# Optimization experiments

Measured on AMD Instinct MI355X. Metric: run time of the kernel, lower is better.

## Reference

```python
import jax, jax.numpy as jnp
import numpy as np

D, H, F, Z = 768, 12, 2048, 100   # d_model, nhead, dim_feedforward, d_z
NL = 2                            # num enc layers == num dec layers
RATIO = 0.05                      # filter_ratio
EPS = 1e-5


def _ln(x, g, b):
    m = x.mean(-1, keepdims=True)
    v = ((x - m) ** 2).mean(-1, keepdims=True)
    return (x - m) / jnp.sqrt(v + EPS) * g + b


def _mha(x, bias, qkv_w, qkv_b, out_w, out_b):
    # x: [N, L, D] (torch seq-first: seq=N responses, batch=L token positions)
    # bias: [L, N] float key-padding mask, ADDED to logits (torch float-mask semantics)
    N, L, _ = x.shape
    hd = D // H
    qkv = jnp.einsum('nld,ed->nle', x, qkv_w) + qkv_b
    q, k, v = jnp.split(qkv, 3, axis=-1)
    q = q.reshape(N, L, H, hd)
    k = k.reshape(N, L, H, hd)
    v = v.reshape(N, L, H, hd)
    scores = jnp.einsum('nlhd,mlhd->lhnm', q, k) / jnp.sqrt(jnp.float32(hd))
    scores = scores + bias[:, None, None, :]
    attn = jax.nn.softmax(scores, axis=-1)
    o = jnp.einsum('lhnm,mlhd->nlhd', attn, v).reshape(N, L, D)
    return o @ out_w.T + out_b


def _stack(x, bias, p):
    qkv_w, qkv_b, out_w, out_b, g1, b1, w1, c1, w2, c2, g2, b2 = p
    for i in range(NL):  # post-norm TransformerEncoderLayer, relu FFN, eval (no dropout)
        a = _mha(x, bias, qkv_w[i], qkv_b[i], out_w[i], out_b[i])
        x = _ln(x + a, g1[i], b1[i])
        f = jax.nn.relu(x @ w1[i].T + c1[i]) @ w2[i].T + c2[i]
        x = _ln(x + f, g2[i], b2[i])
    return x


def _anomaly_scores(emb, msk, enc_p, dec_p, pe_w, pe_b, pd_w, pd_b):
    bias = msk.T  # [L, N]
    h = _stack(emb, bias, enc_p)
    z = jnp.tanh(h @ pe_w.T + pe_b)
    zd = jnp.tanh(z @ pd_w.T + pd_b)
    d = _stack(zd, bias, dec_p)
    # per-response MSE between mean decoded and mean input embedding, summed over D
    return ((d.mean(axis=1) - emb.mean(axis=1)) ** 2).sum(-1)


def _forward(tree_lens, inputs_embeds, attention_mask, enc_p, dec_p, pe_w, pe_b, pd_w, pd_b):
    B, T, L, _ = inputs_embeds.shape
    tls = np.asarray(tree_lens)
    n_resp = tls - 1
    # pack ragged replies: rows 1..tree_len-1 of every tree -> [Ntot, L, D]
    b_idx = np.concatenate([np.full(n, b) for b, n in enumerate(n_resp)])
    t_idx = np.concatenate([np.arange(1, tl) for tl in tls])
    reply = inputs_embeds[b_idx, t_idx]
    masks = attention_mask[b_idx, t_idx]
    s = _anomaly_scores(reply, masks, enc_p, dec_p, pe_w, pe_b, pd_w, pd_b)  # [Ntot]
    Ntot = s.shape[0]
    # original: rank_idx = global_argsort filtered to indices < n_resp[b] (min is always 0)
    # == argsort of the FIRST n_resp[b] packed scores (faithful to the source's indexing)
    masked = jnp.where(jnp.arange(Ntot)[None, :] < jnp.asarray(n_resp)[:, None],
                       s[None, :], jnp.inf)
    order = jnp.argsort(masked, axis=1)[:, :T - 1]  # [B, T-1]
    n_ext = np.maximum(np.floor(n_resp * RATIO).astype(np.int64), 1)
    sel = np.arange(T - 1)[None, :] < n_ext[:, None]          # [B, T-1]
    selj = jnp.asarray(sel)
    node_idx = jnp.where(selj, order + 1, 0)                  # pad slots reuse src (node 0)
    node_full = jnp.concatenate([jnp.zeros((B, 1), node_idx.dtype), node_idx], axis=1)
    brow = jnp.arange(B)[:, None]
    new_emb = inputs_embeds[brow, node_full]                  # [B, T, L, D]
    valid = jnp.asarray(np.concatenate([np.ones((B, 1), bool), sel], axis=1)
                        ).astype(attention_mask.dtype)
    new_msk = attention_mask[brow, node_full] * valid[:, :, None]  # pad rows get zero mask
    ohidx = jnp.where(selj, order + 1, T)                     # dump masked scatters to col T
    oh = jnp.zeros((B, T + 1), jnp.int32).at[brow, ohidx].set(1)[:, :T].at[:, 0].set(1)
    ext_mask = jnp.repeat(oh[:, :, None], L, axis=2).reshape(B, T * L)
    new_tree_lens = jnp.asarray(1 + n_ext, dtype=jnp.int32)
    n_ext_adv = 0
    return oh, ext_mask, n_ext_adv, new_tree_lens, new_emb, new_msk


def setup_inputs() -> dict:
    B, T, L = 16, 32, 64
    key = jax.random.key(0)
    ks = list(jax.random.split(key, 4))
    inp = {
        'tree_lens': jax.random.randint(ks[0], (B,), T // 2, T + 1),
        'inputs_embeds': jax.random.normal(ks[1], (B, T, L, D), jnp.float32),
        'attention_mask': jnp.ones((B, T, L), jnp.float32),
    }
    kit = iter(jax.random.split(ks[2], 32))
    def w(shape):
        return jax.random.normal(next(kit), (NL,) + shape, jnp.float32) * 0.02
    for pre in ('enc', 'dec'):
        inp[pre + '_qkv_w'] = w((3 * D, D)); inp[pre + '_qkv_b'] = jnp.zeros((NL, 3 * D))
        inp[pre + '_out_w'] = w((D, D));     inp[pre + '_out_b'] = jnp.zeros((NL, D))
        inp[pre + '_ln1_g'] = jnp.ones((NL, D)); inp[pre + '_ln1_b'] = jnp.zeros((NL, D))
        inp[pre + '_w1'] = w((F, D)); inp[pre + '_c1'] = jnp.zeros((NL, F))
        inp[pre + '_w2'] = w((D, F)); inp[pre + '_c2'] = jnp.zeros((NL, D))
        inp[pre + '_ln2_g'] = jnp.ones((NL, D)); inp[pre + '_ln2_b'] = jnp.zeros((NL, D))
    inp['pe_w'] = jax.random.normal(next(kit), (Z, D), jnp.float32) * 0.02
    inp['pe_b'] = jnp.zeros((Z,), jnp.float32)
    inp['pd_w'] = jax.random.normal(next(kit), (D, Z), jnp.float32) * 0.02
    inp['pd_b'] = jnp.zeros((D,), jnp.float32)
    return inp


def reference(tree_lens, inputs_embeds, attention_mask,
              enc_qkv_w, enc_qkv_b, enc_out_w, enc_out_b, enc_ln1_g, enc_ln1_b,
              enc_w1, enc_c1, enc_w2, enc_c2, enc_ln2_g, enc_ln2_b,
              dec_qkv_w, dec_qkv_b, dec_out_w, dec_out_b, dec_ln1_g, dec_ln1_b,
              dec_w1, dec_c1, dec_w2, dec_c2, dec_ln2_g, dec_ln2_b,
              pe_w, pe_b, pd_w, pd_b):
    enc_p = (enc_qkv_w, enc_qkv_b, enc_out_w, enc_out_b, enc_ln1_g, enc_ln1_b,
             enc_w1, enc_c1, enc_w2, enc_c2, enc_ln2_g, enc_ln2_b)
    dec_p = (dec_qkv_w, dec_qkv_b, dec_out_w, dec_out_b, dec_ln1_g, dec_ln1_b,
             dec_w1, dec_c1, dec_w2, dec_c2, dec_ln2_g, dec_ln2_b)
    return _forward(tree_lens, inputs_embeds, attention_mask, enc_p, dec_p,
                    pe_w, pe_b, pd_w, pd_b)
```

## Files before the change

kernel.cpp:

```cpp
#include <hip/hip_runtime.h>
#include <hip/hip_bf16.h>
#include <math.h>


#define B_  16
#define T_  32
#define L_  64
#define D_  768
#define H_  12
#define F_  2048
#define ZR_ 100
#define NP_ 512
#define EPS_ 1e-5f

#define MI_NTOT  0
#define MI_NRESP 8
#define MI_OFF   32
#define MI_BIDX  64
#define MI_TIDX  576
#define MI_NODE  1088

#define WS_BIAS2 2048
#define WS_EMEAN 34816
#define WS_S     428032
#define WS_WST   428544
#define WS_BIG   1313280

#define PEB_F    (WS_WST + 196608)

#define OUT_OH   0
#define OUT_EXT  512
#define OUT_NEA  33280
#define OUT_NTL  33281
#define OUT_NEMB 33297
#define OUT_NMSK 25199121
#define OUT_XSCR 33300
#define OUT_WSTK 12616224

#define WSEG0 1769472
#define WSEG1 589824
#define WSEG2 1572864
#define WSEG3 1572864
#define WPASS 5505024

typedef __attribute__((ext_vector_type(8))) short short8;
typedef __attribute__((ext_vector_type(4))) float f32x4;

__device__ inline float bf2f(unsigned s) {
  return __uint_as_float((s & 0xffffu) << 16);
}
__device__ inline unsigned short f2bf(float x) {
  unsigned u = __float_as_uint(x);
  u += 0x7fffu + ((u >> 16) & 1u);
  return (unsigned short)(u >> 16);
}
__device__ inline unsigned pack2(float a, float b) {
  return (unsigned)f2bf(a) | ((unsigned)f2bf(b) << 16);
}

__global__ void meta_kernel(const int* __restrict__ tl, int* __restrict__ mi) {
  if (threadIdx.x != 0) return;
  int off = 0;
  for (int b = 0; b < B_; b++) {
    int nr = tl[b] - 1;
    mi[MI_NRESP + b] = nr;
    mi[MI_OFF + b] = off;
    off += nr;
  }
  mi[MI_NTOT] = off;
  for (int j = 0; j < NP_; j++) {
    int b = -1, t = 0;
    if (j < off) {
      b = 0;
      while (b + 1 < B_ && j >= mi[MI_OFF + b + 1]) b++;
      t = j - mi[MI_OFF + b] + 1;
    }
    mi[MI_BIDX + j] = b;
    mi[MI_TIDX + j] = t;
  }
}

__global__ __launch_bounds__(256) void w2bf4_kernel(
    const float* __restrict__ s0, const float* __restrict__ s1,
    const float* __restrict__ s2, const float* __restrict__ s3,
    unsigned short* __restrict__ dst) {
  const int e = blockIdx.x * 1024 + threadIdx.x * 4;
  const float* src;
  int off;
  if (e < WSEG0)                         { src = s0; off = e; }
  else if (e < WSEG0 + WSEG1)            { src = s1; off = e - WSEG0; }
  else if (e < WSEG0 + WSEG1 + WSEG2)    { src = s2; off = e - WSEG0 - WSEG1; }
  else                                   { src = s3; off = e - WSEG0 - WSEG1 - WSEG2; }
  float4 v = *(const float4*)(src + off);
  uint2 pk; pk.x = pack2(v.x, v.y); pk.y = pack2(v.z, v.w);
  *(uint2*)(dst + e) = pk;
}

__global__ __launch_bounds__(256) void pepd_stage(
    const float* __restrict__ pew, const float* __restrict__ peb,
    const float* __restrict__ pdw,
    unsigned short* __restrict__ dpe, unsigned short* __restrict__ dpd,
    float* __restrict__ dpeb) {
  const int blk = blockIdx.x, t = threadIdx.x;
  if (blk < 192) {
    const int e = blk * 1024 + t * 4;
    const int r = e / 768, c = e % 768;
    float v[4];
    #pragma unroll
    for (int j = 0; j < 4; j++) v[j] = (r < ZR_) ? pew[r * 768 + c + j] : 0.f;
    uint2 pk; pk.x = pack2(v[0], v[1]); pk.y = pack2(v[2], v[3]);
    *(uint2*)(dpe + e) = pk;
  } else if (blk < 384) {
    const int e = (blk - 192) * 1024 + t * 4;
    const int r = e / 256, c = e % 256;
    float v[4];
    #pragma unroll
    for (int j = 0; j < 4; j++) v[j] = (c + j < ZR_) ? pdw[r * ZR_ + c + j] : 0.f;
    uint2 pk; pk.x = pack2(v[0], v[1]); pk.y = pack2(v[2], v[3]);
    *(uint2*)(dpd + e) = pk;
  } else {
    dpeb[t] = (t < ZR_) ? peb[t] : 0.f;
  }
}

__global__ __launch_bounds__(192) void gather_kernel(
    const float* __restrict__ emb, const float* __restrict__ am,
    const int* __restrict__ mi, unsigned short* __restrict__ X,
    float* __restrict__ bias2) {
  const int blk = blockIdx.x;
  const int j = blk >> 6, l = blk & 63;
  const int ntot = mi[MI_NTOT];
  const int t = threadIdx.x;
  float4 v = make_float4(0.f, 0.f, 0.f, 0.f);
  if (j < ntot) {
    const int b = mi[MI_BIDX + j], tt = mi[MI_TIDX + j];
    v = ((const float4*)(emb + (size_t)((b * T_ + tt) * L_ + l) * D_))[t];
    if (t == 0) bias2[blk] = am[(b * T_ + tt) * L_ + l];
  } else {
    if (t == 0) bias2[blk] = -1e30f;
  }
  uint2 pk; pk.x = pack2(v.x, v.y); pk.y = pack2(v.z, v.w);
  *(uint2*)(X + (size_t)blk * D_ + t * 4) = pk;
}

__global__ __launch_bounds__(256) void zerotail_kernel(const int* __restrict__ mi,
                                                       unsigned short* __restrict__ BIG) {
  const int row = blockIdx.x;
  if (row < mi[MI_NTOT] * 64) return;
  uint4 z = make_uint4(0u, 0u, 0u, 0u);
  uint4* p = (uint4*)(BIG + (size_t)row * 2304);
  for (int c = threadIdx.x; c < 288; c += 256) p[c] = z;
}

__global__ __launch_bounds__(256) void emean_kernel(const unsigned short* __restrict__ X,
                                                    float* __restrict__ em) {
  const int j = blockIdx.x;
  int d = threadIdx.x;
  for (int c = 0; c < 3; c++, d += 256) {
    const unsigned short* p = X + (size_t)j * L_ * D_ + d;
    float s = 0.f;
    for (int l = 0; l < L_; l++) s += bf2f(p[l * D_]);
    em[j * D_ + d] = s * (1.f / 64.f);
  }
}

__device__ inline float blockSum256(float v, float* red) {
  #pragma unroll
  for (int o = 32; o > 0; o >>= 1) v += __shfl_down(v, o);
  const int lane = threadIdx.x & 63, wid = threadIdx.x >> 6;
  __syncthreads();
  if (lane == 0) red[wid] = v;
  __syncthreads();
  return red[0] + red[1] + red[2] + red[3];
}

__global__ __launch_bounds__(256) void ln_kernel(unsigned short* __restrict__ X,
                                                 const float* __restrict__ g,
                                                 const float* __restrict__ bb,
                                                 const int* __restrict__ mi) {
  const int row = blockIdx.x;
  if (row >= mi[MI_NTOT] * L_) return;
  unsigned short* p = X + (size_t)row * D_;
  const int t = threadIdx.x;
  __shared__ float red[4];
  float v0 = bf2f(p[t]), v1 = bf2f(p[t + 256]), v2 = bf2f(p[t + 512]);
  float s = blockSum256(v0 + v1 + v2, red);
  float m = s * (1.f / 768.f);
  float d0 = v0 - m, d1 = v1 - m, d2 = v2 - m;
  float q = blockSum256(d0 * d0 + d1 * d1 + d2 * d2, red);
  float r = rsqrtf(q * (1.f / 768.f) + EPS_);
  p[t]       = f2bf(d0 * r * g[t]       + bb[t]);
  p[t + 256] = f2bf(d1 * r * g[t + 256] + bb[t + 256]);
  p[t + 512] = f2bf(d2 * r * g[t + 512] + bb[t + 512]);
}

template <int ACT, bool ADD>
__global__ __launch_bounds__(512, 2) void gemm_mfma(
    const unsigned short* __restrict__ A, int lda, int K,
    const unsigned short* __restrict__ W, int ldw,
    const float* __restrict__ bias,
    unsigned short* __restrict__ C, int ldc, int CT,
    const int* __restrict__ mi) {
  const int rows = mi[MI_NTOT] * 64;
  const int RTa = (rows + 255) >> 8;
  const int NTa = RTa * CT;
  const int id = blockIdx.x;
  if (id >= NTa) return;
  const int q8 = NTa >> 3, r8 = NTa & 7;
  const int xcd = id & 7, idx = id >> 3;
  const int wg = (xcd < r8 ? xcd * (q8 + 1) : r8 * (q8 + 1) + (xcd - r8) * q8) + idx;
  const int row0 = (wg / CT) * 256;
  const int col0 = (wg % CT) * 256;
  __shared__ unsigned short As[2][256 * 32];
  __shared__ unsigned short Bs[2][256 * 32];
  const int t = threadIdx.x;
  const int lane = t & 63, w = t >> 6;
  const int wr = w >> 2, wc = w & 3;
  const int quad = lane >> 4, l15 = lane & 15;

  const int srow = t >> 2;
  const int sgs = (t & 3) ^ ((srow >> 1) & 3);
  const unsigned short* aSrc = A + (size_t)(row0 + srow) * lda + sgs * 8;
  const unsigned short* bSrc = W + (size_t)(col0 + srow) * ldw + sgs * 8;

#define STAGE_(ph, kk, Ad, Bd)                                                  \
  do {                                                                          \
    __builtin_amdgcn_global_load_lds(                                           \
        (const __attribute__((address_space(1))) void*)(aSrc + (size_t)(ph) * 128 * lda + (kk)), \
        (__attribute__((address_space(3))) void*)((Ad) + (ph) * 4096 + w * 512), 16, 0, 0); \
    __builtin_amdgcn_global_load_lds(                                           \
        (const __attribute__((address_space(1))) void*)(bSrc + (size_t)(ph) * 128 * ldw + (kk)), \
        (__attribute__((address_space(3))) void*)((Bd) + (ph) * 4096 + w * 512), 16, 0, 0); \
  } while (0)

  auto LDA_ = [&](const unsigned short* buf, int m) -> short8 {
    const int ar = wr * 128 + m * 16 + l15;
    return *(const short8*)(buf + ar * 32 + (quad ^ ((ar >> 1) & 3)) * 8);
  };
  auto LDB_ = [&](const unsigned short* buf, int n) -> short8 {
    const int bn = wc * 64 + n * 16 + l15;
    return *(const short8*)(buf + bn * 32 + (quad ^ ((bn >> 1) & 3)) * 8);
  };

  f32x4 acc[8][4];
  #pragma unroll
  for (int m = 0; m < 8; m++)
    #pragma unroll
    for (int n = 0; n < 4; n++) acc[m][n] = (f32x4){0.f, 0.f, 0.f, 0.f};

  STAGE_(0, 0, As[0], Bs[0]);
  STAGE_(1, 0, As[0], Bs[0]);
  __syncthreads();

  const int KT = K >> 5;
  for (int kt = 0; kt < KT; ++kt) {
    const unsigned short* Ac = As[kt & 1];
    const unsigned short* Bc = Bs[kt & 1];
    unsigned short* An = As[(kt + 1) & 1];
    unsigned short* Bn = Bs[(kt + 1) & 1];
    const int kn = (kt + 1) << 5;
    const bool more = kn < K;
    short8 afr[4], bfr[4];

    #pragma unroll
    for (int n = 0; n < 4; n++) bfr[n] = LDB_(Bc, n);
    #pragma unroll
    for (int m = 0; m < 4; m++) afr[m] = LDA_(Ac, m);
    if (more) STAGE_(0, kn, An, Bn);
    __builtin_amdgcn_s_setprio(1);
    #pragma unroll
    for (int m = 0; m < 4; m++)
      #pragma unroll
      for (int n = 0; n < 4; n++)
        acc[m][n] = __builtin_amdgcn_mfma_f32_16x16x32_bf16(afr[m], bfr[n], acc[m][n], 0, 0, 0);
    __builtin_amdgcn_s_setprio(0);

    #pragma unroll
    for (int m = 0; m < 4; m++) afr[m] = LDA_(Ac, m + 4);
    if (more) STAGE_(1, kn, An, Bn);
    __builtin_amdgcn_s_setprio(1);
    #pragma unroll
    for (int m = 0; m < 4; m++)
      #pragma unroll
      for (int n = 0; n < 4; n++)
        acc[m + 4][n] = __builtin_amdgcn_mfma_f32_16x16x32_bf16(afr[m], bfr[n], acc[m + 4][n], 0, 0, 0);
    __builtin_amdgcn_s_setprio(0);

    __syncthreads();
  }
#undef STAGE_

  float bv[4];
  #pragma unroll
  for (int n = 0; n < 4; n++) bv[n] = bias[col0 + wc * 64 + n * 16 + l15];
  #pragma unroll
  for (int m = 0; m < 8; m++) {
    #pragma unroll
    for (int reg = 0; reg < 4; reg++) {
      const size_t cr = (size_t)(row0 + wr * 128 + m * 16 + quad * 4 + reg) * ldc;
      #pragma unroll
      for (int n = 0; n < 4; n++) {
        const int cn = col0 + wc * 64 + n * 16 + l15;
        float x = acc[m][n][reg] + bv[n];
        if (ACT == 1) x = fmaxf(x, 0.f);
        if (ACT == 2) x = tanhf(x);
        if (ADD) x += bf2f(C[cr + cn]);
        C[cr + cn] = f2bf(x);
      }
    }
  }
}

__global__ __launch_bounds__(512) void attn_kernel(
    unsigned short* __restrict__ QKV, const float* __restrict__ bias2,
    const int* __restrict__ mi) {
  const int ntot = mi[MI_NTOT];
  const int id = blockIdx.x;
  const int xcd = id & 7, rr = id >> 3;
  const int ntp = rr & 3, lhi = rr >> 2;
  if (ntp * 128 >= ntot) return;
  const int lh = lhi * 8 + xcd;
  const int l = lh / H_, h = lh - l * H_;
  __shared__ unsigned short QPs[128 * 64];
  __shared__ unsigned short Ks0[64 * 64], Ks1[64 * 64];
  __shared__ unsigned short Vt0[64 * 64], Vt1[64 * 64];
  __shared__ float Bls[512];
  const int t = threadIdx.x;
  const int lane = t & 63, w = t >> 6;
  const int quad = lane >> 4, l15 = lane & 15;
  const int q0 = ntp * 128;
  const size_t TSTRIDE = (size_t)64 * L_ * 2304;

  const int krow = t >> 3;
  const int kgs = (t & 7) ^ (krow & 7);
  const unsigned short* ksrc =
      QKV + (size_t)(krow * L_ + l) * 2304 + 768 + h * 64 + kgs * 8;
  const unsigned short* vsrc =
      QKV + (size_t)(lane * L_ + l) * 2304 + 1536 + h * 64 + w * 8;

  auto stageK = [&](int mt, unsigned short* Kw) {
    __builtin_amdgcn_global_load_lds(
        (const __attribute__((address_space(1))) void*)(ksrc + (size_t)mt * TSTRIDE),
        (__attribute__((address_space(3))) void*)(Kw + w * 512), 16, 0, 0);
  };
  auto scatterV = [&](uint4 a0, unsigned short* Vw) {
    const unsigned short* p0 = (const unsigned short*)&a0;
    #pragma unroll
    for (int j = 0; j < 8; j++) {
      const int d = w * 8 + j;
      Vw[d * 64 + ((lane >> 3) ^ (d & 7)) * 8 + (lane & 7)] = p0[j];
    }
  };

  #pragma unroll
  for (int r = 0; r < 2; r++) {
    const int c = r * 512 + t;
    const int row = c >> 3, g = c & 7, gs = g ^ (row & 7);
    const unsigned short* gq =
        QKV + (size_t)((q0 + row) * L_ + l) * 2304 + h * 64 + gs * 8;
    __builtin_amdgcn_global_load_lds(
        (const __attribute__((address_space(1))) void*)gq,
        (__attribute__((address_space(3))) void*)(QPs + r * 4096 + w * 512), 16, 0, 0);
  }
  stageK(0, Ks0);
  uint4 pv0 = *(const uint4*)vsrc;
  Bls[t] = bias2[t * 64 + l];
  __syncthreads();

  const int qrow = w * 16 + l15;
  short8 aq[2];
  #pragma unroll
  for (int kq = 0; kq < 2; kq++)
    aq[kq] = *(const short8*)(QPs + qrow * 64 + ((kq * 4 + quad) ^ (qrow & 7)) * 8);
  scatterV(pv0, Vt0);
  __syncthreads();

  float runmax = -3.0e38f, runsum = 0.f;
  f32x4 oacc[4];
  #pragma unroll
  for (int i = 0; i < 4; i++) oacc[i] = (f32x4){0.f, 0.f, 0.f, 0.f};

  auto tilecomp = [&](int mt, const unsigned short* Krd, const unsigned short* Vrd) {
    f32x4 sa[4];
    #pragma unroll
    for (int n = 0; n < 4; n++) sa[n] = (f32x4){0.f, 0.f, 0.f, 0.f};
    __builtin_amdgcn_s_setprio(1);
    #pragma unroll
    for (int n = 0; n < 4; n++) {
      const int kr = n * 16 + l15;
      #pragma unroll
      for (int kq = 0; kq < 2; kq++) {
        const short8 bk = *(const short8*)(Krd + kr * 64 + ((kq * 4 + quad) ^ (kr & 7)) * 8);
        sa[n] = __builtin_amdgcn_mfma_f32_16x16x32_bf16(bk, aq[kq], sa[n], 0, 0, 0);
      }
    }
    __builtin_amdgcn_s_setprio(0);
    #pragma unroll
    for (int n = 0; n < 4; n++) {
      const float4 bj = *(const float4*)(Bls + mt * 64 + n * 16 + quad * 4);
      sa[n][0] = sa[n][0] * 0.125f + bj.x;
      sa[n][1] = sa[n][1] * 0.125f + bj.y;
      sa[n][2] = sa[n][2] * 0.125f + bj.z;
      sa[n][3] = sa[n][3] * 0.125f + bj.w;
    }

    float m16 = -3.0e38f;
    #pragma unroll
    for (int n = 0; n < 4; n++)
      m16 = fmaxf(m16, fmaxf(fmaxf(sa[n][0], sa[n][1]), fmaxf(sa[n][2], sa[n][3])));
    m16 = fmaxf(m16, __shfl_xor(m16, 16));
    m16 = fmaxf(m16, __shfl_xor(m16, 32));
    const float nm = fmaxf(runmax, m16);
    const float alpha = __expf(runmax - nm);
    runmax = nm;
    float s16 = 0.f;
    #pragma unroll
    for (int n = 0; n < 4; n++)
      #pragma unroll
      for (int reg = 0; reg < 4; reg++) {
        const float p = __expf(sa[n][reg] - nm);
        sa[n][reg] = p; s16 += p;
      }
    s16 += __shfl_xor(s16, 16);
    s16 += __shfl_xor(s16, 32);
    runsum = runsum * alpha + s16;
    float al[4];
    #pragma unroll
    for (int reg = 0; reg < 4; reg++)
      al[reg] = __shfl(alpha, (lane & 48) | (quad * 4 + reg));
    #pragma unroll
    for (int dn = 0; dn < 4; dn++)
      #pragma unroll
      for (int reg = 0; reg < 4; reg++) oacc[dn][reg] *= al[reg];

    #pragma unroll
    for (int n = 0; n < 4; n++)
      #pragma unroll
      for (int reg = 0; reg < 4; reg++) {
        const int key = n * 16 + quad * 4 + reg;
        QPs[qrow * 64 + ((key >> 3) ^ (qrow & 7)) * 8 + (key & 7)] = f2bf(sa[n][reg]);
      }
    short8 ap[2];
    #pragma unroll
    for (int kq = 0; kq < 2; kq++)
      ap[kq] = *(const short8*)(QPs + qrow * 64 + ((kq * 4 + quad) ^ (qrow & 7)) * 8);

    __builtin_amdgcn_s_setprio(1);
    #pragma unroll
    for (int dn = 0; dn < 4; dn++) {
      const int dr = dn * 16 + l15;
      #pragma unroll
      for (int kq = 0; kq < 2; kq++) {
        const short8 bv = *(const short8*)(Vrd + dr * 64 + ((kq * 4 + quad) ^ (dr & 7)) * 8);
        oacc[dn] = __builtin_amdgcn_mfma_f32_16x16x32_bf16(ap[kq], bv, oacc[dn], 0, 0, 0);
      }
    }
    __builtin_amdgcn_s_setprio(0);
  };

  for (int mt2 = 0; mt2 < 8; mt2 += 2) {
    {
      stageK(mt2 + 1, Ks1);
      uint4 n0 = *(const uint4*)(vsrc + (size_t)(mt2 + 1) * TSTRIDE);
      tilecomp(mt2, Ks0, Vt0);
      scatterV(n0, Vt1);
      __syncthreads();
    }
    {
      const bool more = (mt2 + 2) < 8;
      uint4 m0 = make_uint4(0, 0, 0, 0);
      if (more) {
        stageK(mt2 + 2, Ks0);
        m0 = *(const uint4*)(vsrc + (size_t)(mt2 + 2) * TSTRIDE);
      }
      tilecomp(mt2 + 1, Ks1, Vt1);
      if (more) scatterV(m0, Vt0);
      __syncthreads();
    }
  }

  const float inv = 1.f / runsum;
  float iv[4];
  #pragma unroll
  for (int reg = 0; reg < 4; reg++)
    iv[reg] = __shfl(inv, (lane & 48) | (quad * 4 + reg));
  #pragma unroll
  for (int reg = 0; reg < 4; reg++) {
    const int q = q0 + w * 16 + quad * 4 + reg;
    unsigned short* op = QKV + (size_t)(q * L_ + l) * 2304 + h * 64;
    #pragma unroll
    for (int dn = 0; dn < 4; dn++)
      op[dn * 16 + l15] = f2bf(oacc[dn][reg] * iv[reg]);
  }
}

__global__ __launch_bounds__(256) void score_kernel(const unsigned short* __restrict__ X,
                                                    const float* __restrict__ em,
                                                    float* __restrict__ Sv) {
  const int j = blockIdx.x;
  const int t = threadIdx.x;
  __shared__ float red[4];
  float part = 0.f;
  for (int c = 0; c < 3; c++) {
    const int d = t + c * 256;
    const unsigned short* p = X + (size_t)j * L_ * D_ + d;
    float s = 0.f;
    for (int l = 0; l < L_; l++) s += bf2f(p[l * D_]);
    const float diff = s * (1.f / 64.f) - em[j * D_ + d];
    part += diff * diff;
  }
  const float tot = blockSum256(part, red);
  if (t == 0) Sv[j] = tot;
}

__global__ __launch_bounds__(256) void finalize_kernel(const float* __restrict__ Sv,
                                                       int* __restrict__ mi,
                                                       float* __restrict__ out) {
  const int t = threadIdx.x;
  if (t < B_) {
    const int nr = mi[MI_NRESP + t];
    float best = 3.0e38f; int bi = 0;
    for (int j = 0; j < nr; j++) {
      const float v = Sv[j];
      if (v < best) { best = v; bi = j; }
    }
    mi[MI_NODE + t] = bi + 1;
    int next = nr / 20; if (next < 1) next = 1;
    out[OUT_NTL + t] = (float)(1 + next);
  }
  if (t == 0) out[OUT_NEA] = 0.f;
  __syncthreads();
  for (int idx = t; idx < B_ * T_; idx += 256) {
    const int b = idx >> 5, tt = idx & 31;
    out[OUT_OH + idx] = (tt == 0 || tt == mi[MI_NODE + b]) ? 1.f : 0.f;
  }
}

__global__ __launch_bounds__(256) void maskout_kernel(const float* __restrict__ am,
                                                      const int* __restrict__ mi,
                                                      float* __restrict__ out) {
  const int idx = blockIdx.x * 256 + threadIdx.x;
  const int b = idx >> 11, rem = idx & 2047;
  const int tt = rem >> 6, l = rem & 63;
  const int node = mi[MI_NODE + b];
  out[OUT_EXT + idx] = (tt == 0 || tt == node) ? 1.f : 0.f;
  float nm;
  if (tt == 0)      nm = am[(b * T_) * L_ + l];
  else if (tt == 1) nm = am[(b * T_ + node) * L_ + l];
  else              nm = 0.f;
  out[OUT_NMSK + idx] = nm;
}

__global__ __launch_bounds__(192) void newemb_kernel(const float* __restrict__ emb,
                                                     const int* __restrict__ mi,
                                                     float* __restrict__ out) {
  const int blk = blockIdx.x;
  const int b = blk >> 11, rem = blk & 2047;
  const int tt = rem >> 6, l = rem & 63;
  const int srct = (tt == 1) ? mi[MI_NODE + b] : 0;
  const float4 v = ((const float4*)(emb + (size_t)((b * T_ + srct) * L_ + l) * D_))[threadIdx.x];
  float* dst = out + OUT_NEMB + (size_t)blk * D_ + threadIdx.x * 4;
  dst[0] = v.x; dst[1] = v.y; dst[2] = v.z; dst[3] = v.w;
}

extern "C" void kernel_launch(void* const* d_in, const int* in_sizes, int n_in,
                              void* d_out, int out_size, void* d_ws, size_t ws_size,
                              hipStream_t stream) {
  (void)in_sizes; (void)n_in; (void)out_size; (void)ws_size;
  const int*   tl  = (const int*)d_in[0];
  const float* emb = (const float*)d_in[1];
  const float* am  = (const float*)d_in[2];
  const float* P[28];
  for (int i = 0; i < 28; i++) P[i] = (const float*)d_in[3 + i];

  float* wsf   = (float*)d_ws;
  int*   mi    = (int*)d_ws;
  float* bias2 = wsf + WS_BIAS2;
  float* emean = wsf + WS_EMEAN;
  float* Sv    = wsf + WS_S;
  unsigned short* Wst = (unsigned short*)(wsf + WS_WST);
  unsigned short* peW = Wst;
  unsigned short* pdW = Wst + 196608;
  float* peB   = wsf + PEB_F;
  unsigned short* BIG = (unsigned short*)(wsf + WS_BIG);
  unsigned short* Zs  = (unsigned short*)(wsf + WS_BIG);
  float* out   = (float*)d_out;
  unsigned short* X    = (unsigned short*)(out + OUT_XSCR);
  unsigned short* WSTK = (unsigned short*)(out + OUT_WSTK);

  meta_kernel<<<1, 64, 0, stream>>>(tl, mi);
  for (int p = 0; p < 4; p++) {
    const float* const* q = P + (p >> 1) * 12;
    const int i = p & 1;
    w2bf4_kernel<<<WPASS / 1024, 256, 0, stream>>>(
        q[0] + (size_t)i * 3 * D_ * D_, q[2] + (size_t)i * D_ * D_,
        q[6] + (size_t)i * F_ * D_, q[8] + (size_t)i * D_ * F_,
        WSTK + (size_t)p * WPASS);
  }
  pepd_stage<<<385, 256, 0, stream>>>(P[24], P[25], P[26], peW, pdW, peB);
  gather_kernel<<<NP_ * L_, 192, 0, stream>>>(emb, am, mi, X, bias2);
  emean_kernel<<<NP_, 256, 0, stream>>>(X, emean);
  zerotail_kernel<<<NP_ * L_, 256, 0, stream>>>(mi, BIG);

  const int RT2 = NP_ * 64 / 256;
  for (int s = 0; s < 2; s++) {
    const float* const* q = P + s * 12;
    for (int i = 0; i < 2; i++) {
      const unsigned short* WP = WSTK + (size_t)(s * 2 + i) * WPASS;
      gemm_mfma<0, false><<<RT2 * 9, 512, 0, stream>>>(
          X, D_, D_, WP, D_, q[1] + i * 3 * D_, BIG, 3 * D_, 9, mi);
      attn_kernel<<<L_ * H_ * 4, 512, 0, stream>>>(BIG, bias2, mi);
      gemm_mfma<0, true><<<RT2 * 3, 512, 0, stream>>>(
          BIG, 3 * D_, D_, WP + WSEG0, D_, q[3] + i * D_, X, D_, 3, mi);
      ln_kernel<<<NP_ * L_, 256, 0, stream>>>(X, q[4] + i * D_, q[5] + i * D_, mi);
      gemm_mfma<1, false><<<RT2 * 8, 512, 0, stream>>>(
          X, D_, D_, WP + WSEG0 + WSEG1, D_, q[7] + i * F_, BIG, F_, 8, mi);
      gemm_mfma<0, true><<<RT2 * 3, 512, 0, stream>>>(
          BIG, F_, F_, WP + WSEG0 + WSEG1 + WSEG2, F_, q[9] + i * D_, X, D_, 3, mi);
      ln_kernel<<<NP_ * L_, 256, 0, stream>>>(X, q[10] + i * D_, q[11] + i * D_, mi);
    }
    if (s == 0) {
      gemm_mfma<2, false><<<RT2 * 1, 512, 0, stream>>>(
          X, D_, D_, peW, D_, peB, Zs, 256, 1, mi);
      gemm_mfma<2, false><<<RT2 * 3, 512, 0, stream>>>(
          Zs, 256, 256, pdW, 256, P[27], X, D_, 3, mi);
    }
  }

  score_kernel<<<NP_, 256, 0, stream>>>(X, emean, Sv);
  finalize_kernel<<<1, 256, 0, stream>>>(Sv, mi, out);
  maskout_kernel<<<128, 256, 0, stream>>>(am, mi, out);
  newemb_kernel<<<B_ * T_ * L_, 192, 0, stream>>>(emb, mi, out);
}
```

Baseline: 2.867 ms.

## Triple-buffer GEMM LDS staging with two-tile prefetch and partial vmcnt waits

The bf16 MFMA GEMM moves from double to triple LDS buffering, so global-to-LDS loads run two K-tiles ahead. The full __syncthreads is replaced by an explicit s_waitcnt vmcnt(4) plus s_barrier, which lets the newest prefetch stay in flight across the barrier. The aim is to hide global load latency behind MFMA work. In exchange, LDS use grows to 96 KB per block, which may limit the two-blocks-per-CU occupancy the launch bounds request.

```diff
diff --git a/kernel.cpp b/kernel.cpp
--- a/kernel.cpp
+++ b/kernel.cpp
@@ -211,8 +211,8 @@
   const int wg = (xcd < r8 ? xcd * (q8 + 1) : r8 * (q8 + 1) + (xcd - r8) * q8) + idx;
   const int row0 = (wg / CT) * 256;
   const int col0 = (wg % CT) * 256;
-  __shared__ unsigned short As[2][256 * 32];
-  __shared__ unsigned short Bs[2][256 * 32];
+  __shared__ unsigned short As[3][256 * 32];
+  __shared__ unsigned short Bs[3][256 * 32];
   const int t = threadIdx.x;
   const int lane = t & 63, w = t >> 6;
   const int wr = w >> 2, wc = w & 3;
@@ -248,25 +248,30 @@
     #pragma unroll
     for (int n = 0; n < 4; n++) acc[m][n] = (f32x4){0.f, 0.f, 0.f, 0.f};
 
-  STAGE_(0, 0, As[0], Bs[0]);
-  STAGE_(1, 0, As[0], Bs[0]);
-  __syncthreads();
+  unsigned short* a0 = As[0]; unsigned short* a1 = As[1]; unsigned short* a2 = As[2];
+  unsigned short* b0 = Bs[0]; unsigned short* b1 = Bs[1]; unsigned short* b2 = Bs[2];
+
+  STAGE_(0, 0, a0, b0);
+  STAGE_(1, 0, a0, b0);
+  STAGE_(0, 32, a1, b1);
+  STAGE_(1, 32, a1, b1);
+  __builtin_amdgcn_sched_barrier(0);
+  asm volatile("s_waitcnt vmcnt(4)" ::: "memory");
+  __builtin_amdgcn_sched_barrier(0);
+  __builtin_amdgcn_s_barrier();
+  __builtin_amdgcn_sched_barrier(0);
 
   const int KT = K >> 5;
   for (int kt = 0; kt < KT; ++kt) {
-    const unsigned short* Ac = As[kt & 1];
-    const unsigned short* Bc = Bs[kt & 1];
-    unsigned short* An = As[(kt + 1) & 1];
-    unsigned short* Bn = Bs[(kt + 1) & 1];
-    const int kn = (kt + 1) << 5;
-    const bool more = kn < K;
+    const bool m2 = (kt + 2) < KT;
+    const int kn = (kt + 2) << 5;
     short8 afr[4], bfr[4];
 
     #pragma unroll
-    for (int n = 0; n < 4; n++) bfr[n] = LDB_(Bc, n);
-    #pragma unroll
-    for (int m = 0; m < 4; m++) afr[m] = LDA_(Ac, m);
-    if (more) STAGE_(0, kn, An, Bn);
+    for (int n = 0; n < 4; n++) bfr[n] = LDB_(b0, n);
+    #pragma unroll
+    for (int m = 0; m < 4; m++) afr[m] = LDA_(a0, m);
+    if (m2) STAGE_(0, kn, a2, b2);
     __builtin_amdgcn_s_setprio(1);
     #pragma unroll
     for (int m = 0; m < 4; m++)
@@ -276,8 +281,8 @@
     __builtin_amdgcn_s_setprio(0);
 
     #pragma unroll
-    for (int m = 0; m < 4; m++) afr[m] = LDA_(Ac, m + 4);
-    if (more) STAGE_(1, kn, An, Bn);
+    for (int m = 0; m < 4; m++) afr[m] = LDA_(a0, m + 4);
+    if (m2) STAGE_(1, kn, a2, b2);
     __builtin_amdgcn_s_setprio(1);
     #pragma unroll
     for (int m = 0; m < 4; m++)
@@ -286,7 +291,16 @@
         acc[m + 4][n] = __builtin_amdgcn_mfma_f32_16x16x32_bf16(afr[m], bfr[n], acc[m + 4][n], 0, 0, 0);
     __builtin_amdgcn_s_setprio(0);
 
-    __syncthreads();
+    if (kt + 1 < KT) {
+      __builtin_amdgcn_sched_barrier(0);
+      if (m2) asm volatile("s_waitcnt vmcnt(4)" ::: "memory");
+      else    asm volatile("s_waitcnt vmcnt(0)" ::: "memory");
+      __builtin_amdgcn_sched_barrier(0);
+      __builtin_amdgcn_s_barrier();
+      __builtin_amdgcn_sched_barrier(0);
+    }
+    unsigned short* ta = a0; a0 = a1; a1 = a2; a2 = ta;
+    unsigned short* tb = b0; b0 = b1; b1 = b2; b2 = tb;
   }
 #undef STAGE_
 
```

Measured after the change: 2.700 ms. 1.06x faster.
